# Performance work log

Hardware: AMD Instinct MI355X
Metric: run time of the kernel (lower is better)

## Reference

```python
import jax, jax.numpy as jnp
import numpy as np

B, N, F, H, K, HID, TAB = 4, 256, 1024, 16, 128, 4096, 32
D = F // H
PI = 3.14159  # matches literal in source


def setup_inputs() -> dict:
    key = jax.random.key(0)
    ks = jax.random.split(key, 20)
    r = lambda i, shape: jax.random.normal(ks[i], shape, jnp.float32) * 0.02
    return dict(
        nfeat=jax.random.normal(ks[0], (B, N, F), jnp.float32),
        sp_dist=jax.random.randint(ks[1], (B, N, N), 0, TAB, dtype=jnp.int32),
        rd_dist=jax.random.uniform(ks[2], (B, N, N), jnp.float32),
        dist_table=r(3, (TAB, K)),
        g_means=jax.random.uniform(ks[4], (K,), jnp.float32, 0.0, 3.0),
        g_stds=jax.random.uniform(ks[5], (K,), jnp.float32, 0.0, 3.0),
        g_mul=jnp.ones((1,), jnp.float32),
        g_bias=jnp.zeros((1,), jnp.float32),
        mlp_w1=r(6, (2 * K, H)), mlp_b1=jnp.zeros((H,), jnp.float32),
        mlp_w2=r(7, (H, H)), mlp_b2=jnp.zeros((H,), jnp.float32),
        wq=r(8, (F, F)), bq=jnp.zeros((F,), jnp.float32),
        wk=r(9, (F, F)), bk=jnp.zeros((F,), jnp.float32),
        wv=r(10, (F, F)), bv=jnp.zeros((F,), jnp.float32),
        wo=r(11, (F, F)), bo=jnp.zeros((F,), jnp.float32),
        ffn_w1=r(12, (F, HID)), ffn_b1=jnp.zeros((HID,), jnp.float32),
        ffn_w2=r(13, (HID, F)), ffn_b2=jnp.zeros((F,), jnp.float32),
        ln1_g=jnp.ones((F,), jnp.float32), ln1_b=jnp.zeros((F,), jnp.float32),
        ln2_g=jnp.ones((F,), jnp.float32), ln2_b=jnp.zeros((F,), jnp.float32),
    )


def _layer_norm(x, g, b):
    m = x.mean(-1, keepdims=True)
    v = ((x - m) ** 2).mean(-1, keepdims=True)
    return (x - m) / jnp.sqrt(v + 1e-5) * g + b


def reference(nfeat, sp_dist, rd_dist, dist_table, g_means, g_stds, g_mul, g_bias,
              mlp_w1, mlp_b1, mlp_w2, mlp_b2, wq, bq, wk, bk, wv, bv, wo, bo,
              ffn_w1, ffn_b1, ffn_w2, ffn_b2, ln1_g, ln1_b, ln2_g, ln2_b):
    # --- FusedDistEncoder: shortest-path embedding + Gaussian resistance-distance encoding ---
    sp_emb = dist_table[sp_dist]                      # [B,N,N,K]
    x = g_mul * rd_dist[..., None] + g_bias           # [B,N,N,1] -> broadcast over K
    std = jnp.abs(g_stds) + 0.01                      # [K]
    rd_emb = jnp.exp(-0.5 * ((x - g_means) / std) ** 2) / (((2 * PI) ** 0.5) * std)
    h = jnp.concatenate([sp_emb, rd_emb], axis=-1)    # [B,N,N,2K]
    h = jax.nn.gelu(h @ mlp_w1 + mlp_b1, approximate=False)
    attn_bias = h @ mlp_w2 + mlp_b2                   # [B,N,N,H]

    # --- BiasedMultiheadAttention (note: source divides q by scaling=d^-0.5, i.e. *sqrt(d)) ---
    q = (nfeat @ wq + bq).reshape(B, N, H, D) * (D ** 0.5)
    k = (nfeat @ wk + bk).reshape(B, N, H, D)
    v = (nfeat @ wv + bv).reshape(B, N, H, D)
    scores = jnp.einsum('bihd,bjhd->bijh', q, k) + attn_bias   # [B,N,N,H]
    w = jax.nn.softmax(scores, axis=2)                          # softmax over key dim j
    attn = jnp.einsum('bijh,bjhd->bihd', w, v).reshape(B, N, F) @ wo + bo

    # --- GraphormerLayer residuals (post-norm, dropout=0 / eval) ---
    x1 = _layer_norm(nfeat + attn, ln1_g, ln1_b)
    ffn = jax.nn.relu(x1 @ ffn_w1 + ffn_b1) @ ffn_w2 + ffn_b2
    return _layer_norm(x1 + ffn, ln2_g, ln2_b)
```

## Files before the change

### kernel.cpp

```cpp
#include <hip/hip_runtime.h>
#include <hip/hip_bf16.h>
#include <math.h>

typedef __hip_bfloat16 bf16;
typedef float f32x4 __attribute__((ext_vector_type(4)));
typedef short bf16x8 __attribute__((ext_vector_type(8)));

#define AS1 __attribute__((address_space(1)))
#define AS3 __attribute__((address_space(3)))

__global__ __launch_bounds__(256) void setup_kernel(
    const float* __restrict__ nfeat, bf16* __restrict__ nfeatb,
    const float* __restrict__ bq, const float* __restrict__ bk,
    const float* __restrict__ bv, float* __restrict__ bqkv,
    const float* __restrict__ table, const float* __restrict__ w1,
    float* __restrict__ tw)
{
    int bid = blockIdx.x, t = threadIdx.x;
    if (bid < 1024) {
        int i = (bid * 256 + t) * 4;
        float4 v = *reinterpret_cast<const float4*>(nfeat + i);
        nfeatb[i + 0] = (bf16)v.x; nfeatb[i + 1] = (bf16)v.y;
        nfeatb[i + 2] = (bf16)v.z; nfeatb[i + 3] = (bf16)v.w;
    } else if (bid < 1036) {
        int i = (bid - 1024) * 256 + t;
        bqkv[i] = i < 1024 ? bq[i] : (i < 2048 ? bk[i - 1024] : bv[i - 2048]);
    } else {
        #pragma unroll
        for (int e = t; e < 512; e += 256) {
            int r = e >> 4, o = e & 15;
            float a = 0.f;
            for (int k = 0; k < 128; ++k) a += table[r * 128 + k] * w1[k * 16 + o];
            tw[e] = a;
        }
    }
}

__global__ __launch_bounds__(256) void wt_all_kernel(
    const float* __restrict__ wq, const float* __restrict__ wk,
    const float* __restrict__ wv, const float* __restrict__ wo,
    const float* __restrict__ fw1, const float* __restrict__ fw2,
    bf16* __restrict__ qkvT, bf16* __restrict__ woT,
    bf16* __restrict__ fw1T, bf16* __restrict__ fw2T)
{
    __shared__ float tile[32][33];
    int bid = blockIdx.x, t = threadIdx.x;
    const float* W; bf16* WT; int Kd, Nd, local;
    if (bid < 3072)      { int ws = bid >> 10; local = bid & 1023;
                           W = ws == 0 ? wq : ws == 1 ? wk : wv;
                           WT = qkvT + ws * 1048576; Kd = 1024; Nd = 1024; }
    else if (bid < 4096) { local = bid - 3072; W = wo;  WT = woT;  Kd = 1024; Nd = 1024; }
    else if (bid < 8192) { local = bid - 4096; W = fw1; WT = fw1T; Kd = 1024; Nd = 4096; }
    else                 { local = bid - 8192; W = fw2; WT = fw2T; Kd = 4096; Nd = 1024; }
    int ntn = Nd >> 5;
    int n0 = (local % ntn) * 32, k0 = (local / ntn) * 32;
    int tx = t & 31, ty = t >> 5;
    #pragma unroll
    for (int p = 0; p < 4; p++)
        tile[ty + p * 8][tx] = W[(k0 + ty + p * 8) * Nd + n0 + tx];
    __syncthreads();
    #pragma unroll
    for (int p = 0; p < 4; p++)
        WT[(n0 + ty + p * 8) * Kd + k0 + tx] = (bf16)tile[tx][ty + p * 8];
}

__global__ __launch_bounds__(256) void enc_kernel(
    const int* __restrict__ sp, const float* __restrict__ rd,
    const float* __restrict__ tw,
    const float* __restrict__ means, const float* __restrict__ stds,
    const float* __restrict__ gmul, const float* __restrict__ gbias,
    const float* __restrict__ w1, const float* __restrict__ b1,
    const float* __restrict__ w2, const float* __restrict__ b2,
    bf16* __restrict__ biasT)
{
    __shared__ float w1s[128][16];
    __shared__ float w2s[16][16];
    __shared__ float b1s[16], b2s[16];
    __shared__ float meanS[128], istdS[128], coefS[128];
    int t = threadIdx.x;
    for (int i = t; i < 2048; i += 256) w1s[i >> 4][i & 15] = w1[2048 + i];
    w2s[t >> 4][t & 15] = w2[t];
    if (t < 16) { b1s[t] = b1[t]; b2s[t] = b2[t]; }
    if (t < 128) {
        float s = fabsf(stds[t]) + 0.01f;
        meanS[t] = means[t];
        istdS[t] = 1.f / s;
        coefS[t] = 1.f / (sqrtf(2.f * 3.14159f) * s);
    }
    __syncthreads();

    int p = blockIdx.x * 256 + t;
    int idx = sp[p];
    float xv = gmul[0] * rd[p] + gbias[0];

    float acc[16];
    #pragma unroll
    for (int o = 0; o < 16; o++) acc[o] = b1s[o] + tw[idx * 16 + o];

    for (int k = 0; k < 128; k++) {
        float d = (xv - meanS[k]) * istdS[k];
        float g = coefS[k] * __expf(-0.5f * d * d);
        #pragma unroll
        for (int o = 0; o < 16; o++) acc[o] += g * w1s[k][o];
    }
    float h[16];
    #pragma unroll
    for (int o = 0; o < 16; o++) {
        float a = acc[o];
        h[o] = 0.5f * a * (1.f + erff(a * 0.70710678118f));
    }
    float outv[16];
    #pragma unroll
    for (int o = 0; o < 16; o++) outv[o] = b2s[o];
    #pragma unroll
    for (int q = 0; q < 16; q++) {
        float hq = h[q];
        #pragma unroll
        for (int o = 0; o < 16; o++) outv[o] += hq * w2s[q][o];
    }
    int b = blockIdx.x >> 8, i = blockIdx.x & 255;
    #pragma unroll
    for (int hh = 0; hh < 16; hh++)
        biasT[(((b * 16 + hh) * 256 + i) << 8) + t] = (bf16)outv[hh];
}

__global__ __launch_bounds__(256, 4) void gemm_bf16(
    const bf16* __restrict__ A, const bf16* __restrict__ BT,
    const float* __restrict__ bias, const float* __restrict__ add,
    void* __restrict__ C, int M, int Nd, int Kd, int epi)
{
    __shared__ __align__(16) char smem[32768];
    int t = threadIdx.x;
    int w = t >> 6, l = t & 63;
    int wr = w >> 1, wc = w & 1;
    int lr = l & 15, hi = l >> 4;
    int row0 = blockIdx.y * 64, col0 = blockIdx.x * 64;
    int nz = gridDim.z;
    int klen = Kd / nz;
    int kbeg = blockIdx.z * klen;

    f32x4 acc[2][2];
    #pragma unroll
    for (int i = 0; i < 2; i++)
        #pragma unroll
        for (int j = 0; j < 2; j++) acc[i][j] = (f32x4){0.f, 0.f, 0.f, 0.f};

    const bf16* Asrc = A + (row0 + (t & 63)) * Kd + kbeg + (t >> 6) * 8;
    const bf16* Bsrc = BT + (col0 + (t & 63)) * Kd + kbeg + (t >> 6) * 8;
    int wbase = (t & 192) * 16;

    #pragma unroll
    for (int p = 0; p < 2; p++) {
        __builtin_amdgcn_global_load_lds((const AS1 void*)(Asrc + p * 32),
                                         (AS3 void*)(smem + p * 4096 + wbase), 16, 0, 0);
        __builtin_amdgcn_global_load_lds((const AS1 void*)(Bsrc + p * 32),
                                         (AS3 void*)(smem + 8192 + p * 4096 + wbase), 16, 0, 0);
    }
    __syncthreads();

    int nsteps = klen >> 6;
    int cur = 0;
    for (int s = 0; s < nsteps; ++s) {
        int nxt = cur ^ 1;
        if (s + 1 < nsteps) {
            const bf16* An = Asrc + (s + 1) * 64;
            const bf16* Bn = Bsrc + (s + 1) * 64;
            #pragma unroll
            for (int p = 0; p < 2; p++) {
                __builtin_amdgcn_global_load_lds((const AS1 void*)(An + p * 32),
                    (AS3 void*)(smem + nxt * 16384 + p * 4096 + wbase), 16, 0, 0);
                __builtin_amdgcn_global_load_lds((const AS1 void*)(Bn + p * 32),
                    (AS3 void*)(smem + nxt * 16384 + 8192 + p * 4096 + wbase), 16, 0, 0);
            }
        }
        const char* base = smem + cur * 16384;
        bf16x8 af[2][2], bfr[2][2];
        #pragma unroll
        for (int kk = 0; kk < 2; kk++) {
            #pragma unroll
            for (int mi = 0; mi < 2; mi++)
                af[kk][mi] = *(const bf16x8*)(base + kk * 4096 + hi * 1024 +
                                              (wr * 32 + mi * 16 + lr) * 16);
            #pragma unroll
            for (int nj = 0; nj < 2; nj++)
                bfr[kk][nj] = *(const bf16x8*)(base + 8192 + kk * 4096 + hi * 1024 +
                                               (wc * 32 + nj * 16 + lr) * 16);
        }
        #pragma unroll
        for (int kk = 0; kk < 2; kk++)
            #pragma unroll
            for (int mi = 0; mi < 2; mi++)
                #pragma unroll
                for (int nj = 0; nj < 2; nj++)
                    acc[mi][nj] = __builtin_amdgcn_mfma_f32_16x16x32_bf16(
                        af[kk][mi], bfr[kk][nj], acc[mi][nj], 0, 0, 0);
        __syncthreads();
        cur = nxt;
    }

    if (nz > 1) {
        float* P = (float*)C + (size_t)blockIdx.z * M * Nd;
        #pragma unroll
        for (int i = 0; i < 2; i++) {
            int rb = row0 + wr * 32 + i * 16 + hi * 4;
            #pragma unroll
            for (int j = 0; j < 2; j++) {
                int cc = col0 + wc * 32 + j * 16 + lr;
                f32x4 v = acc[i][j];
                #pragma unroll
                for (int q = 0; q < 4; q++) P[(rb + q) * Nd + cc] = v[q];
            }
        }
        return;
    }

    #pragma unroll
    for (int i = 0; i < 2; i++) {
        int rb = row0 + wr * 32 + i * 16 + hi * 4;
        #pragma unroll
        for (int j = 0; j < 2; j++) {
            int cc = col0 + wc * 32 + j * 16 + lr;
            float bsv = bias[cc];
            f32x4 v = acc[i][j];
            #pragma unroll
            for (int q = 0; q < 4; q++) {
                int r = rb + q;
                float x = v[q] + bsv;
                if (epi == 0) {
                    ((float*)C)[r * Nd + cc] = x;
                } else if (epi == 1) {
                    ((float*)C)[r * Nd + cc] = x + add[r * Nd + cc];
                } else if (epi == 2) {
                    ((bf16*)C)[r * Nd + cc] = (bf16)fmaxf(x, 0.f);
                } else {
                    bf16* Cb = (bf16*)C;
                    int sel = cc >> 10, ccc = cc & 1023;
                    int hh = ccc >> 6, dd = ccc & 63;
                    int bb = r >> 8, ii = r & 255;
                    if (sel == 0)
                        Cb[(((bb * 16 + hh) * 256 + ii) << 6) + dd] = (bf16)(x * 8.0f);
                    else if (sel == 1)
                        Cb[1048576 + (((bb * 16 + hh) * 256 + ii) << 6) + dd] = (bf16)x;
                    else
                        Cb[2097152 + ((((bb * 16 + hh) << 6) + dd) << 8) + ii] = (bf16)x;
                }
            }
        }
    }
}

__global__ __launch_bounds__(256) void flash_kernel(
    const bf16* __restrict__ Qb, const bf16* __restrict__ Kb,
    const bf16* __restrict__ VT, const bf16* __restrict__ biasT,
    bf16* __restrict__ out)
{
    __shared__ __align__(16) char pls[32768];
    int t = threadIdx.x;
    int w = t >> 6, l = t & 63;
    int lr = l & 15, hi = l >> 4;
    int bh = blockIdx.x >> 2, iq = blockIdx.x & 3;
    int b = bh >> 4, h = bh & 15;
    int i0 = iq * 64 + w * 16;

    const bf16* Qp = Qb + (bh * 256 + i0 + lr) * 64 + hi * 8;
    bf16x8 qf0 = *(const bf16x8*)(Qp);
    bf16x8 qf1 = *(const bf16x8*)(Qp + 32);

    f32x4 acc[16];
    #pragma unroll
    for (int f = 0; f < 16; f++) acc[f] = (f32x4){0.f, 0.f, 0.f, 0.f};

    const bf16* Kp = Kb + (bh * 256 + lr) * 64 + hi * 8;
    #pragma unroll
    for (int f = 0; f < 16; f++) {
        bf16x8 kf0 = *(const bf16x8*)(Kp + f * 1024);
        bf16x8 kf1 = *(const bf16x8*)(Kp + f * 1024 + 32);
        acc[f] = __builtin_amdgcn_mfma_f32_16x16x32_bf16(qf0, kf0, acc[f], 0, 0, 0);
        acc[f] = __builtin_amdgcn_mfma_f32_16x16x32_bf16(qf1, kf1, acc[f], 0, 0, 0);
    }

    const bf16* bp = biasT + (bh * 256 + i0 + hi * 4) * 256 + lr;
    #pragma unroll
    for (int f = 0; f < 16; f++)
        #pragma unroll
        for (int q = 0; q < 4; q++)
            acc[f][q] += __bfloat162float(bp[q * 256 + f * 16]);

    float inv[4];
    #pragma unroll
    for (int q = 0; q < 4; q++) {
        float m = acc[0][q];
        #pragma unroll
        for (int f = 1; f < 16; f++) m = fmaxf(m, acc[f][q]);
        #pragma unroll
        for (int msk = 1; msk < 16; msk <<= 1) m = fmaxf(m, __shfl_xor(m, msk));
        float s = 0.f;
        #pragma unroll
        for (int f = 0; f < 16; f++) {
            float e = __expf(acc[f][q] - m);
            acc[f][q] = e;
            s += e;
        }
        #pragma unroll
        for (int msk = 1; msk < 16; msk <<= 1) s += __shfl_xor(s, msk);
        inv[q] = 1.f / s;
    }

    char* Pw = pls + w * 8192;
    #pragma unroll
    for (int f = 0; f < 16; f++) {
        int j = f * 16 + lr;
        int c = j >> 3, jo = j & 7;
        #pragma unroll
        for (int q = 0; q < 4; q++)
            *(bf16*)(Pw + c * 256 + (hi * 4 + q) * 16 + jo * 2) = (bf16)(acc[f][q] * inv[q]);
    }
    __syncthreads();

    const char* Pr = pls + w * 8192 + hi * 256 + lr * 16;
    const bf16* Vp = VT + (bh * 64 + lr) * 256 + hi * 8;
    #pragma unroll
    for (int n = 0; n < 4; n++) {
        f32x4 o = (f32x4){0.f, 0.f, 0.f, 0.f};
        #pragma unroll
        for (int ks = 0; ks < 8; ks++) {
            bf16x8 pa = *(const bf16x8*)(Pr + ks * 1024);
            bf16x8 vb = *(const bf16x8*)(Vp + n * 4096 + ks * 32);
            o = __builtin_amdgcn_mfma_f32_16x16x32_bf16(pa, vb, o, 0, 0, 0);
        }
        #pragma unroll
        for (int q = 0; q < 4; q++)
            out[(b * 256 + i0 + hi * 4 + q) * 1024 + h * 64 + n * 16 + lr] = (bf16)o[q];
    }
}

__global__ __launch_bounds__(256) void ln_fused_kernel(
    const float* __restrict__ part, int S,
    const float* __restrict__ bias, const float* __restrict__ add,
    const float* __restrict__ g, const float* __restrict__ bta,
    float* __restrict__ out, bf16* __restrict__ ob)
{
    int row = blockIdx.x;
    int t = threadIdx.x;
    float v[4];
    float sum = 0.f;
    #pragma unroll
    for (int i = 0; i < 4; i++) {
        int c = t + i * 256;
        float x = add[row * 1024 + c] + bias[c];
        for (int s = 0; s < S; s++) x += part[s * 1048576 + row * 1024 + c];
        v[i] = x;
        sum += x;
    }
    __shared__ float red[8];
    #pragma unroll
    for (int off = 32; off; off >>= 1) sum += __shfl_xor(sum, off);
    if ((t & 63) == 0) red[t >> 6] = sum;
    __syncthreads();
    float mean = (red[0] + red[1] + red[2] + red[3]) * (1.f / 1024.f);
    float vs = 0.f;
    #pragma unroll
    for (int i = 0; i < 4; i++) { float d = v[i] - mean; vs += d * d; }
    #pragma unroll
    for (int off = 32; off; off >>= 1) vs += __shfl_xor(vs, off);
    if ((t & 63) == 0) red[4 + (t >> 6)] = vs;
    __syncthreads();
    float var = (red[4] + red[5] + red[6] + red[7]) * (1.f / 1024.f);
    float invs = rsqrtf(var + 1e-5f);
    #pragma unroll
    for (int i = 0; i < 4; i++) {
        int c = t + i * 256;
        float o = (v[i] - mean) * invs * g[c] + bta[c];
        out[row * 1024 + c] = o;
        if (ob) ob[row * 1024 + c] = (bf16)o;
    }
}

extern "C" void kernel_launch(void* const* d_in, const int* in_sizes, int n_in,
                              void* d_out, int out_size, void* d_ws, size_t ws_size,
                              hipStream_t stream)
{
    const float* nfeat  = (const float*)d_in[0];
    const int*   sp     = (const int*)  d_in[1];
    const float* rd     = (const float*)d_in[2];
    const float* table  = (const float*)d_in[3];
    const float* gmeans = (const float*)d_in[4];
    const float* gstds  = (const float*)d_in[5];
    const float* gmul   = (const float*)d_in[6];
    const float* gbias  = (const float*)d_in[7];
    const float* w1     = (const float*)d_in[8];
    const float* b1     = (const float*)d_in[9];
    const float* w2     = (const float*)d_in[10];
    const float* b2     = (const float*)d_in[11];
    const float* wq     = (const float*)d_in[12];
    const float* bq     = (const float*)d_in[13];
    const float* wk     = (const float*)d_in[14];
    const float* bk     = (const float*)d_in[15];
    const float* wv     = (const float*)d_in[16];
    const float* bv     = (const float*)d_in[17];
    const float* wo     = (const float*)d_in[18];
    const float* bo     = (const float*)d_in[19];
    const float* fw1    = (const float*)d_in[20];
    const float* fb1    = (const float*)d_in[21];
    const float* fw2    = (const float*)d_in[22];
    const float* fb2    = (const float*)d_in[23];
    const float* ln1g   = (const float*)d_in[24];
    const float* ln1b   = (const float*)d_in[25];
    const float* ln2g   = (const float*)d_in[26];
    const float* ln2b   = (const float*)d_in[27];

    const size_t MB = 1 << 20;
    char* cws = (char*)d_ws;
    bf16*  biasT   = (bf16*)(cws);
    bf16*  qkvb    = (bf16*)(cws + 8 * MB);
    float* part    = (float*)(cws + 8 * MB);
    bf16*  qkvT    = (bf16*)(cws + 16 * MB);
    bf16*  woT     = (bf16*)(cws + 22 * MB);
    bf16*  fw1T    = (bf16*)(cws + 24 * MB);
    bf16*  fw2T    = (bf16*)(cws + 32 * MB);
    float* x1      = (float*)(cws + 40 * MB);
    bf16*  nfeatb  = (bf16*)(cws + 44 * MB);
    bf16*  x1b     = (bf16*)(cws + 46 * MB);
    bf16*  attnob  = (bf16*)(cws + 48 * MB);
    float* bqkv    = (float*)(cws + 50 * MB);
    float* tw      = (float*)(cws + 50 * MB + 16384);
    bf16*  hiddenb = biasT;

    setup_kernel<<<1037, 256, 0, stream>>>(nfeat, nfeatb, bq, bk, bv, bqkv,
                                           table, w1, tw);
    wt_all_kernel<<<12288, 256, 0, stream>>>(wq, wk, wv, wo, fw1, fw2,
                                             qkvT, woT, fw1T, fw2T);
    enc_kernel<<<1024, 256, 0, stream>>>(sp, rd, tw, gmeans, gstds, gmul, gbias,
                                         w1, b1, w2, b2, biasT);

    gemm_bf16<<<dim3(48, 16), 256, 0, stream>>>(nfeatb, qkvT, bqkv, nullptr, qkvb,
                                                1024, 3072, 1024, 3);

    flash_kernel<<<256, 256, 0, stream>>>(qkvb, qkvb + 1048576, qkvb + 2097152,
                                          biasT, attnob);

    gemm_bf16<<<dim3(16, 16, 2), 256, 0, stream>>>(attnob, woT, bo, nullptr, part,
                                                   1024, 1024, 1024, 0);
    ln_fused_kernel<<<1024, 256, 0, stream>>>(part, 2, bo, nfeat, ln1g, ln1b, x1, x1b);

    gemm_bf16<<<dim3(64, 16), 256, 0, stream>>>(x1b, fw1T, fb1, nullptr, hiddenb,
                                                1024, 4096, 1024, 2);

    gemm_bf16<<<dim3(16, 16, 4), 256, 0, stream>>>(hiddenb, fw2T, fb2, nullptr, part,
                                                   1024, 1024, 4096, 0);
    ln_fused_kernel<<<1024, 256, 0, stream>>>(part, 4, fb2, x1, ln2g, ln2b,
                                              (float*)d_out, nullptr);
}
```

Measured before the change: 194.8 us.

## Merge weight transpose and encoder kernels; use explicit waitcnt barriers in GEMM

After: 208.9 us. +7.2%, slower.

```diff
diff --git a/kernel.cpp b/kernel.cpp
--- a/kernel.cpp
+++ b/kernel.cpp
@@ -8,6 +8,11 @@
 
 #define AS1 __attribute__((address_space(1)))
 #define AS3 __attribute__((address_space(3)))
+
+#define ASM_VMCNT4 asm volatile("s_waitcnt vmcnt(4)" ::: "memory")
+#define ASM_VMCNT0 asm volatile("s_waitcnt vmcnt(0)" ::: "memory")
+#define ASM_LGKM0  asm volatile("s_waitcnt lgkmcnt(0)" ::: "memory")
+#define ASM_BARRIER asm volatile("s_barrier" ::: "memory")
 
 __global__ __launch_bounds__(256) void setup_kernel(
     const float* __restrict__ nfeat, bf16* __restrict__ nfeatb,
@@ -36,35 +41,20 @@
     }
 }
 
-__global__ __launch_bounds__(256) void wt_all_kernel(
+struct EncSm {
+    float w1s[128][16];
+    float w2s[16][16];
+    float b1s[16], b2s[16];
+    float meanS[128], istdS[128], coefS[128];
+};
+struct WtSm { float tile[32][33]; };
+
+__global__ __launch_bounds__(256) void prep_kernel(
     const float* __restrict__ wq, const float* __restrict__ wk,
     const float* __restrict__ wv, const float* __restrict__ wo,
     const float* __restrict__ fw1, const float* __restrict__ fw2,
     bf16* __restrict__ qkvT, bf16* __restrict__ woT,
-    bf16* __restrict__ fw1T, bf16* __restrict__ fw2T)
-{
-    __shared__ float tile[32][33];
-    int bid = blockIdx.x, t = threadIdx.x;
-    const float* W; bf16* WT; int Kd, Nd, local;
-    if (bid < 3072)      { int ws = bid >> 10; local = bid & 1023;
-                           W = ws == 0 ? wq : ws == 1 ? wk : wv;
-                           WT = qkvT + ws * 1048576; Kd = 1024; Nd = 1024; }
-    else if (bid < 4096) { local = bid - 3072; W = wo;  WT = woT;  Kd = 1024; Nd = 1024; }
-    else if (bid < 8192) { local = bid - 4096; W = fw1; WT = fw1T; Kd = 1024; Nd = 4096; }
-    else                 { local = bid - 8192; W = fw2; WT = fw2T; Kd = 4096; Nd = 1024; }
-    int ntn = Nd >> 5;
-    int n0 = (local % ntn) * 32, k0 = (local / ntn) * 32;
-    int tx = t & 31, ty = t >> 5;
-    #pragma unroll
-    for (int p = 0; p < 4; p++)
-        tile[ty + p * 8][tx] = W[(k0 + ty + p * 8) * Nd + n0 + tx];
-    __syncthreads();
-    #pragma unroll
-    for (int p = 0; p < 4; p++)
-        WT[(n0 + ty + p * 8) * Kd + k0 + tx] = (bf16)tile[tx][ty + p * 8];
-}
-
-__global__ __launch_bounds__(256) void enc_kernel(
+    bf16* __restrict__ fw1T, bf16* __restrict__ fw2T,
     const int* __restrict__ sp, const float* __restrict__ rd,
     const float* __restrict__ tw,
     const float* __restrict__ means, const float* __restrict__ stds,
@@ -73,35 +63,57 @@
     const float* __restrict__ w2, const float* __restrict__ b2,
     bf16* __restrict__ biasT)
 {
-    __shared__ float w1s[128][16];
-    __shared__ float w2s[16][16];
-    __shared__ float b1s[16], b2s[16];
-    __shared__ float meanS[128], istdS[128], coefS[128];
-    int t = threadIdx.x;
-    for (int i = t; i < 2048; i += 256) w1s[i >> 4][i & 15] = w1[2048 + i];
-    w2s[t >> 4][t & 15] = w2[t];
-    if (t < 16) { b1s[t] = b1[t]; b2s[t] = b2[t]; }
+    __shared__ __align__(16) char smraw[sizeof(EncSm)];
+    int bid = blockIdx.x, t = threadIdx.x;
+
+    if (bid < 12288) {
+        WtSm& sm = *(WtSm*)smraw;
+        const float* W; bf16* WT; int Kd, Nd, local;
+        if (bid < 3072)      { int ws = bid >> 10; local = bid & 1023;
+                               W = ws == 0 ? wq : ws == 1 ? wk : wv;
+                               WT = qkvT + ws * 1048576; Kd = 1024; Nd = 1024; }
+        else if (bid < 4096) { local = bid - 3072; W = wo;  WT = woT;  Kd = 1024; Nd = 1024; }
+        else if (bid < 8192) { local = bid - 4096; W = fw1; WT = fw1T; Kd = 1024; Nd = 4096; }
+        else                 { local = bid - 8192; W = fw2; WT = fw2T; Kd = 4096; Nd = 1024; }
+        int ntn = Nd >> 5;
+        int n0 = (local % ntn) * 32, k0 = (local / ntn) * 32;
+        int tx = t & 31, ty = t >> 5;
+        #pragma unroll
+        for (int p = 0; p < 4; p++)
+            sm.tile[ty + p * 8][tx] = W[(k0 + ty + p * 8) * Nd + n0 + tx];
+        __syncthreads();
+        #pragma unroll
+        for (int p = 0; p < 4; p++)
+            WT[(n0 + ty + p * 8) * Kd + k0 + tx] = (bf16)sm.tile[tx][ty + p * 8];
+        return;
+    }
+
+    EncSm& sm = *(EncSm*)smraw;
+    int ebid = bid - 12288;
+    for (int i = t; i < 2048; i += 256) sm.w1s[i >> 4][i & 15] = w1[2048 + i];
+    sm.w2s[t >> 4][t & 15] = w2[t];
+    if (t < 16) { sm.b1s[t] = b1[t]; sm.b2s[t] = b2[t]; }
     if (t < 128) {
         float s = fabsf(stds[t]) + 0.01f;
-        meanS[t] = means[t];
-        istdS[t] = 1.f / s;
-        coefS[t] = 1.f / (sqrtf(2.f * 3.14159f) * s);
+        sm.meanS[t] = means[t];
+        sm.istdS[t] = 1.f / s;
+        sm.coefS[t] = 1.f / (sqrtf(2.f * 3.14159f) * s);
     }
     __syncthreads();
 
-    int p = blockIdx.x * 256 + t;
+    int p = ebid * 256 + t;
     int idx = sp[p];
     float xv = gmul[0] * rd[p] + gbias[0];
 
     float acc[16];
     #pragma unroll
-    for (int o = 0; o < 16; o++) acc[o] = b1s[o] + tw[idx * 16 + o];
+    for (int o = 0; o < 16; o++) acc[o] = sm.b1s[o] + tw[idx * 16 + o];
 
     for (int k = 0; k < 128; k++) {
-        float d = (xv - meanS[k]) * istdS[k];
-        float g = coefS[k] * __expf(-0.5f * d * d);
-        #pragma unroll
-        for (int o = 0; o < 16; o++) acc[o] += g * w1s[k][o];
+        float d = (xv - sm.meanS[k]) * sm.istdS[k];
+        float g = sm.coefS[k] * __expf(-0.5f * d * d);
+        #pragma unroll
+        for (int o = 0; o < 16; o++) acc[o] += g * sm.w1s[k][o];
     }
     float h[16];
     #pragma unroll
@@ -111,14 +123,14 @@
     }
     float outv[16];
     #pragma unroll
-    for (int o = 0; o < 16; o++) outv[o] = b2s[o];
+    for (int o = 0; o < 16; o++) outv[o] = sm.b2s[o];
     #pragma unroll
     for (int q = 0; q < 16; q++) {
         float hq = h[q];
         #pragma unroll
-        for (int o = 0; o < 16; o++) outv[o] += hq * w2s[q][o];
-    }
-    int b = blockIdx.x >> 8, i = blockIdx.x & 255;
+        for (int o = 0; o < 16; o++) outv[o] += hq * sm.w2s[q][o];
+    }
+    int b = ebid >> 8, i = ebid & 255;
     #pragma unroll
     for (int hh = 0; hh < 16; hh++)
         biasT[(((b * 16 + hh) * 256 + i) << 8) + t] = (bf16)outv[hh];
@@ -156,7 +168,6 @@
         __builtin_amdgcn_global_load_lds((const AS1 void*)(Bsrc + p * 32),
                                          (AS3 void*)(smem + 8192 + p * 4096 + wbase), 16, 0, 0);
     }
-    __syncthreads();
 
     int nsteps = klen >> 6;
     int cur = 0;
@@ -172,7 +183,12 @@
                 __builtin_amdgcn_global_load_lds((const AS1 void*)(Bn + p * 32),
                     (AS3 void*)(smem + nxt * 16384 + 8192 + p * 4096 + wbase), 16, 0, 0);
             }
-        }
+            ASM_VMCNT4;
+        } else {
+            ASM_VMCNT0;
+        }
+        ASM_BARRIER;
+
         const char* base = smem + cur * 16384;
         bf16x8 af[2][2], bfr[2][2];
         #pragma unroll
@@ -186,6 +202,10 @@
                 bfr[kk][nj] = *(const bf16x8*)(base + 8192 + kk * 4096 + hi * 1024 +
                                                (wc * 32 + nj * 16 + lr) * 16);
         }
+        ASM_LGKM0;
+        __builtin_amdgcn_sched_barrier(0);
+        ASM_BARRIER;
+        __builtin_amdgcn_s_setprio(1);
         #pragma unroll
         for (int kk = 0; kk < 2; kk++)
             #pragma unroll
@@ -194,7 +214,7 @@
                 for (int nj = 0; nj < 2; nj++)
                     acc[mi][nj] = __builtin_amdgcn_mfma_f32_16x16x32_bf16(
                         af[kk][mi], bfr[kk][nj], acc[mi][nj], 0, 0, 0);
-        __syncthreads();
+        __builtin_amdgcn_s_setprio(0);
         cur = nxt;
     }
 
@@ -428,10 +448,10 @@
 
     setup_kernel<<<1037, 256, 0, stream>>>(nfeat, nfeatb, bq, bk, bv, bqkv,
                                            table, w1, tw);
-    wt_all_kernel<<<12288, 256, 0, stream>>>(wq, wk, wv, wo, fw1, fw2,
-                                             qkvT, woT, fw1T, fw2T);
-    enc_kernel<<<1024, 256, 0, stream>>>(sp, rd, tw, gmeans, gstds, gmul, gbias,
-                                         w1, b1, w2, b2, biasT);
+    prep_kernel<<<13312, 256, 0, stream>>>(wq, wk, wv, wo, fw1, fw2,
+                                           qkvT, woT, fw1T, fw2T,
+                                           sp, rd, tw, gmeans, gstds, gmul, gbias,
+                                           w1, b1, w2, b2, biasT);
 
     gemm_bf16<<<dim3(48, 16), 256, 0, stream>>>(nfeatb, qkvT, bqkv, nullptr, qkvb,
                                                 1024, 3072, 1024, 3);
```

## Widen weight transpose tiles and hand-schedule GEMM waitcnt and barriers

Applied to the files above, without the earlier changes.

Result: no change. 193.3 us (-0.8%).

```diff
diff --git a/kernel.cpp b/kernel.cpp
--- a/kernel.cpp
+++ b/kernel.cpp
@@ -8,6 +8,11 @@
 
 #define AS1 __attribute__((address_space(1)))
 #define AS3 __attribute__((address_space(3)))
+
+#define ASM_VMCNT4 asm volatile("s_waitcnt vmcnt(4)" ::: "memory")
+#define ASM_VMCNT0 asm volatile("s_waitcnt vmcnt(0)" ::: "memory")
+#define ASM_LGKM0  asm volatile("s_waitcnt lgkmcnt(0)" ::: "memory")
+#define ASM_BARRIER asm volatile("s_barrier" ::: "memory")
 
 __global__ __launch_bounds__(256) void setup_kernel(
     const float* __restrict__ nfeat, bf16* __restrict__ nfeatb,
@@ -36,32 +41,56 @@
     }
 }
 
-__global__ __launch_bounds__(256) void wt_all_kernel(
+__global__ __launch_bounds__(256) void wtx_kernel(
     const float* __restrict__ wq, const float* __restrict__ wk,
     const float* __restrict__ wv, const float* __restrict__ wo,
     const float* __restrict__ fw1, const float* __restrict__ fw2,
     bf16* __restrict__ qkvT, bf16* __restrict__ woT,
     bf16* __restrict__ fw1T, bf16* __restrict__ fw2T)
 {
-    __shared__ float tile[32][33];
+    __shared__ float tile[64][68];
     int bid = blockIdx.x, t = threadIdx.x;
     const float* W; bf16* WT; int Kd, Nd, local;
-    if (bid < 3072)      { int ws = bid >> 10; local = bid & 1023;
+    if (bid < 768)       { int ws = bid >> 8; local = bid & 255;
                            W = ws == 0 ? wq : ws == 1 ? wk : wv;
                            WT = qkvT + ws * 1048576; Kd = 1024; Nd = 1024; }
-    else if (bid < 4096) { local = bid - 3072; W = wo;  WT = woT;  Kd = 1024; Nd = 1024; }
-    else if (bid < 8192) { local = bid - 4096; W = fw1; WT = fw1T; Kd = 1024; Nd = 4096; }
-    else                 { local = bid - 8192; W = fw2; WT = fw2T; Kd = 4096; Nd = 1024; }
-    int ntn = Nd >> 5;
-    int n0 = (local % ntn) * 32, k0 = (local / ntn) * 32;
-    int tx = t & 31, ty = t >> 5;
-    #pragma unroll
-    for (int p = 0; p < 4; p++)
-        tile[ty + p * 8][tx] = W[(k0 + ty + p * 8) * Nd + n0 + tx];
+    else if (bid < 1024) { local = bid - 768;  W = wo;  WT = woT;  Kd = 1024; Nd = 1024; }
+    else if (bid < 2048) { local = bid - 1024; W = fw1; WT = fw1T; Kd = 1024; Nd = 4096; }
+    else                 { local = bid - 2048; W = fw2; WT = fw2T; Kd = 4096; Nd = 1024; }
+    int ntn = Nd >> 6;
+    int k0 = (local / ntn) * 64, n0 = (local % ntn) * 64;
+
+    {
+        int k = t >> 2, nb = (t & 3) * 16;
+        const float* src = W + (size_t)(k0 + k) * Nd + n0 + nb;
+        #pragma unroll
+        for (int c = 0; c < 4; c++) {
+            float4 v = *reinterpret_cast<const float4*>(src + c * 4);
+            *reinterpret_cast<float4*>(&tile[k][nb + c * 4]) = v;
+        }
+    }
     __syncthreads();
-    #pragma unroll
-    for (int p = 0; p < 4; p++)
-        WT[(n0 + ty + p * 8) * Kd + k0 + tx] = (bf16)tile[tx][ty + p * 8];
+
+    {
+        int w = t >> 6, l = t & 63;
+        int n = w * 16 + (l >> 2), kb = (l & 3) * 16;
+        bf16x8 o0, o1;
+        #pragma unroll
+        for (int j = 0; j < 8; j++) {
+            union { bf16 b; short s; } u;
+            u.b = (bf16)tile[kb + j][n];
+            o0[j] = u.s;
+        }
+        #pragma unroll
+        for (int j = 0; j < 8; j++) {
+            union { bf16 b; short s; } u;
+            u.b = (bf16)tile[kb + 8 + j][n];
+            o1[j] = u.s;
+        }
+        bf16* dst = WT + (size_t)(n0 + n) * Kd + k0 + kb;
+        *reinterpret_cast<bf16x8*>(dst) = o0;
+        *reinterpret_cast<bf16x8*>(dst + 8) = o1;
+    }
 }
 
 __global__ __launch_bounds__(256) void enc_kernel(
@@ -156,7 +185,6 @@
         __builtin_amdgcn_global_load_lds((const AS1 void*)(Bsrc + p * 32),
                                          (AS3 void*)(smem + 8192 + p * 4096 + wbase), 16, 0, 0);
     }
-    __syncthreads();
 
     int nsteps = klen >> 6;
     int cur = 0;
@@ -172,7 +200,12 @@
                 __builtin_amdgcn_global_load_lds((const AS1 void*)(Bn + p * 32),
                     (AS3 void*)(smem + nxt * 16384 + 8192 + p * 4096 + wbase), 16, 0, 0);
             }
-        }
+            ASM_VMCNT4;
+        } else {
+            ASM_VMCNT0;
+        }
+        ASM_BARRIER;
+
         const char* base = smem + cur * 16384;
         bf16x8 af[2][2], bfr[2][2];
         #pragma unroll
@@ -186,6 +219,10 @@
                 bfr[kk][nj] = *(const bf16x8*)(base + 8192 + kk * 4096 + hi * 1024 +
                                                (wc * 32 + nj * 16 + lr) * 16);
         }
+        ASM_LGKM0;
+        __builtin_amdgcn_sched_barrier(0);
+        ASM_BARRIER;
+        __builtin_amdgcn_s_setprio(1);
         #pragma unroll
         for (int kk = 0; kk < 2; kk++)
             #pragma unroll
@@ -194,7 +231,7 @@
                 for (int nj = 0; nj < 2; nj++)
                     acc[mi][nj] = __builtin_amdgcn_mfma_f32_16x16x32_bf16(
                         af[kk][mi], bfr[kk][nj], acc[mi][nj], 0, 0, 0);
-        __syncthreads();
+        __builtin_amdgcn_s_setprio(0);
         cur = nxt;
     }
 
@@ -428,8 +465,8 @@
 
     setup_kernel<<<1037, 256, 0, stream>>>(nfeat, nfeatb, bq, bk, bv, bqkv,
                                            table, w1, tw);
-    wt_all_kernel<<<12288, 256, 0, stream>>>(wq, wk, wv, wo, fw1, fw2,
-                                             qkvT, woT, fw1T, fw2T);
+    wtx_kernel<<<3072, 256, 0, stream>>>(wq, wk, wv, wo, fw1, fw2,
+                                         qkvT, woT, fw1T, fw2T);
     enc_kernel<<<1024, 256, 0, stream>>>(sp, rd, tw, gmeans, gstds, gmul, gbias,
                                          w1, b1, w2, b2, biasT);
 
```
